# Performance work log

Hardware: AMD Instinct MI355X
Metric: run time of the kernel (lower is better)

Reference implementation:

```python
import jax, jax.numpy as jnp
import numpy as np
import math

B, S, D, H, FF = 2, 2048, 1024, 16, 4096
DH = D // H
EPS = 1e-5


def layernorm(x, g, b):
    mu = jnp.mean(x, axis=-1, keepdims=True)
    var = jnp.mean((x - mu) ** 2, axis=-1, keepdims=True)
    return (x - mu) * jax.lax.rsqrt(var + EPS) * g + b


def setup_inputs() -> dict:
    key = jax.random.key(0)
    ks = jax.random.split(key, 8)
    s = lambda fan_in: 1.0 / math.sqrt(fan_in)
    return {
        "x": jax.random.normal(ks[0], (B, S, D), jnp.float32),
        "attention_mask": jnp.zeros((B, 1, 1, S), jnp.float32),
        "wq": jax.random.uniform(ks[1], (D, D), jnp.float32, -s(D), s(D)),
        "wk": jax.random.uniform(ks[2], (D, D), jnp.float32, -s(D), s(D)),
        "wv": jax.random.uniform(ks[3], (D, D), jnp.float32, -s(D), s(D)),
        "wo": jax.random.uniform(ks[4], (D, D), jnp.float32, -s(D), s(D)),
        "w1": jax.random.uniform(ks[5], (D, FF), jnp.float32, -s(D), s(D)),
        "w2": jax.random.uniform(ks[6], (FF, D), jnp.float32, -s(FF), s(FF)),
        "ln1_g": jnp.ones((D,), jnp.float32),
        "ln1_b": jnp.zeros((D,), jnp.float32),
        "ln2_g": jnp.ones((D,), jnp.float32),
        "ln2_b": jnp.zeros((D,), jnp.float32),
    }


def reference(x, attention_mask, wq, wk, wv, wo, w1, w2, ln1_g, ln1_b, ln2_g, ln2_b):
    # --- attention ResNorm (pre-LN) ---
    y = layernorm(x, ln1_g, ln1_b)
    q = (y @ wq).reshape(B, S, H, DH)
    k = (y @ wk).reshape(B, S, H, DH)
    v = (y @ wv).reshape(B, S, H, DH)
    # NOTE: original scales by sqrt(hidden_dim), not sqrt(head_dim)
    scores = jnp.einsum("bqhd,bkhd->bhqk", q, k) / math.sqrt(D) + attention_mask
    probs = jax.nn.softmax(scores, axis=-1)
    attn = jnp.einsum("bhqk,bkhd->bqhd", probs, v).reshape(B, S, D)
    x = x + attn @ wo
    # --- FFN ResNorm ---
    y = layernorm(x, ln2_g, ln2_b)
    y = jax.nn.gelu(y @ w1, approximate=False) @ w2
    return x + y
```

## Files before the change

### kernel.cpp

```cpp
#include <hip/hip_runtime.h>
#include <hip/hip_bf16.h>
#include <math.h>

#define Bb 2
#define Ss 2048
#define Dd 1024
#define Hh 16
#define FFf 4096
#define EPSf 1e-5f
#define SCALEf 0.03125f
#define LOG2Ef 1.4426950408889634f
#define SCALE2f (SCALEf * LOG2Ef)
#define KSPLIT 2
#define NTILES ((Ss / KSPLIT) / 64)

typedef short s16x8 __attribute__((ext_vector_type(8)));
typedef short s16x4 __attribute__((ext_vector_type(4)));
typedef float f32x4 __attribute__((ext_vector_type(4)));
typedef float f32x16 __attribute__((ext_vector_type(16)));

__device__ __forceinline__ short f2bs(float f) {
    union { float f; unsigned u; } v; v.f = f;
    const unsigned r = (v.u + 0x7FFFu + ((v.u >> 16) & 1u)) >> 16;
    return (short)r;
}
__device__ __forceinline__ float bs2f(short s) {
    union { unsigned u; float f; } v; v.u = ((unsigned)(unsigned short)s) << 16;
    return v.f;
}
__device__ __forceinline__ float gelu_exact(float v) {
    return 0.5f * v * (1.0f + erff(v * 0.7071067811865475f));
}
__device__ __forceinline__ void gload16(const void* g, void* l) {
    __builtin_amdgcn_global_load_lds(
        (const __attribute__((address_space(1))) unsigned int*)g,
        (__attribute__((address_space(3))) unsigned int*)l, 16, 0, 0);
}
__device__ __forceinline__ unsigned cvt_pk(float lo, float hi) {
    unsigned r;
    asm("v_cvt_pk_bf16_f32 %0, %1, %2" : "=v"(r) : "v"(lo), "v"(hi));
    return r;
}

__global__ __launch_bounds__(256) void prep(const float* __restrict__ wq, const float* __restrict__ wk,
                                            const float* __restrict__ wv, const float* __restrict__ wo,
                                            const float* __restrict__ w1, const float* __restrict__ w2,
                                            const float* __restrict__ mask,
                                            short* __restrict__ qkvw_t, short* __restrict__ wot,
                                            short* __restrict__ w1t, short* __restrict__ w2t,
                                            float* __restrict__ msc) {
    const int blk = blockIdx.x;
    const int tid = threadIdx.x;
    if (blk >= 3072) {
#pragma unroll
        for (int j = 0; j < 16; ++j) msc[tid + j * 256] = mask[tid + j * 256] * LOG2Ef;
        return;
    }
    const float* W; short* Wt; int K, N, inner;
    if (blk < 1024) {
        const int which = blk >> 8; inner = blk & 255;
        K = 1024; N = 1024;
        W = (which == 0) ? wq : (which == 1) ? wk : (which == 2) ? wv : wo;
        Wt = (which < 3) ? qkvw_t + (size_t)which * 1024 * 1024 : wot;
    } else if (blk < 2048) {
        inner = blk - 1024; K = 1024; N = 4096; W = w1; Wt = w1t;
    } else {
        inner = blk - 2048; K = 4096; N = 1024; W = w2; Wt = w2t;
    }
    const int nbx = N / 64;
    const int bx = inner % nbx, by = inner / nbx;
    __shared__ short T[64][65];
    const int n0 = bx * 64, k0 = by * 64;
    const int c = tid & 63, rg = tid >> 6;
#pragma unroll
    for (int j = 0; j < 16; ++j) {
        const int r = rg * 16 + j;
        T[r][c] = f2bs(W[(size_t)(k0 + r) * N + n0 + c]);
    }
    __syncthreads();
#pragma unroll
    for (int j = 0; j < 16; ++j) {
        const int r = rg * 16 + j;
        Wt[(size_t)(n0 + r) * K + k0 + c] = T[c][r];
    }
}

__global__ __launch_bounds__(256) void vtranspose(const short* __restrict__ QKV,
                                                  short* __restrict__ VT) {
    __shared__ __align__(16) short T[64 * 144];
    const int t = threadIdx.x;
    const int bh = blockIdx.x;
    const int sc = blockIdx.y;
    const int b = bh >> 4, h = bh & 15;
#pragma unroll
    for (int i = 0; i < 4; ++i) {
        const int sl = i * 32 + (t >> 3);
        const int d0 = (t & 7) * 8;
        const s16x8 v = *(const s16x8*)&QKV[((size_t)(b * Ss + sc * 128 + sl)) * 3072 + 2048 + h * 64 + d0];
#pragma unroll
        for (int e = 0; e < 8; ++e) {
            const int d = d0 + e;
            T[(d * 144 + sl) ^ (((d >> 3) & 7) << 3)] = v[e];
        }
    }
    __syncthreads();
#pragma unroll
    for (int i = 0; i < 4; ++i) {
        const int d = i * 16 + (t >> 4);
        const int s0 = (t & 15) * 8;
        const s16x8 o = *(const s16x8*)&T[(d * 144 + s0) ^ (((d >> 3) & 7) << 3)];
        *(s16x8*)&VT[((size_t)(bh * 64 + d)) * 2048 + sc * 128 + s0] = o;
    }
}

__global__ __launch_bounds__(256) void layernorm_bf16(const float* __restrict__ X,
                                                      const float* __restrict__ g,
                                                      const float* __restrict__ bta,
                                                      short* __restrict__ Y) {
    __shared__ float red[8];
    const int row = blockIdx.x;
    const int tid = threadIdx.x;
    const size_t base = (size_t)row * Dd + tid * 4;
    const float4 xv = *(const float4*)&X[base];
    float s  = xv.x + xv.y + xv.z + xv.w;
    float sq = xv.x * xv.x + xv.y * xv.y + xv.z * xv.z + xv.w * xv.w;
#pragma unroll
    for (int o = 32; o >= 1; o >>= 1) {
        s  += __shfl_xor(s, o, 64);
        sq += __shfl_xor(sq, o, 64);
    }
    const int lane = tid & 63, wv = tid >> 6;
    if (lane == 0) { red[wv] = s; red[4 + wv] = sq; }
    __syncthreads();
    const float tot  = red[0] + red[1] + red[2] + red[3];
    const float totq = red[4] + red[5] + red[6] + red[7];
    const float mu  = tot * (1.0f / Dd);
    const float var = totq * (1.0f / Dd) - mu * mu;
    const float inv = 1.0f / sqrtf(var + EPSf);
    const float4 gv = *(const float4*)&g[tid * 4];
    const float4 bv = *(const float4*)&bta[tid * 4];
    s16x4 o;
    o[0] = f2bs((xv.x - mu) * inv * gv.x + bv.x);
    o[1] = f2bs((xv.y - mu) * inv * gv.y + bv.y);
    o[2] = f2bs((xv.z - mu) * inv * gv.z + bv.z);
    o[3] = f2bs((xv.w - mu) * inv * gv.w + bv.w);
    *(s16x4*)&Y[base] = o;
}

template <int BM, int BN, int BK, int EPI>
__global__ __launch_bounds__(256, 4) void gemm_v4(const short* __restrict__ A,
                                                  const short* __restrict__ Bt,
                                                  const float* __restrict__ R,
                                                  void* __restrict__ Cout,
                                                  int M, int N, int K, int gx) {
    constexpr int WM = BM / 2, WN = BN / 2;
    constexpr int MF = WM / 16, NF = WN / 16;
    constexpr int S   = BK / 8;
    constexpr int LPR = BK / 8;
    constexpr int RPI = 64 / LPR;
    constexpr int IPWA = (BM / 4) / RPI;
    constexpr int IPWB = (BN / 4) / RPI;
    __shared__ __align__(16) short As[2][BM * BK];
    __shared__ __align__(16) short Bs[2][BN * BK];

    const int tid = threadIdx.x;
    const int w = tid >> 6, l = tid & 63;
    const int lr = l & 15, lg = l >> 4;
    const int wr = w >> 1, wc = w & 1;

    const int nwg = gridDim.x;
    const int bid = blockIdx.x;
    const int swz = (bid & 7) * (nwg >> 3) + (bid >> 3);
    const int bx = swz % gx, by = swz / gx;

    const int lrow = l / LPR;
    const int sslot = ((l % LPR) ^ (((lrow * BK) >> 6) & (S - 1))) * 8;
    const size_t arow0 = (size_t)(by * BM);
    const size_t brow0 = (size_t)(bx * BN);

    f32x4 acc[NF][MF] = {};

    auto STAGE = [&](int bi, int k0) {
#pragma unroll
        for (int j = 0; j < IPWA; ++j) {
            const int r0 = w * (BM / 4) + j * RPI;
            gload16(A + (arow0 + r0 + lrow) * K + k0 + sslot, &As[bi][r0 * BK]);
        }
#pragma unroll
        for (int j = 0; j < IPWB; ++j) {
            const int r0 = w * (BN / 4) + j * RPI;
            gload16(Bt + (brow0 + r0 + lrow) * K + k0 + sslot, &Bs[bi][r0 * BK]);
        }
    };

    int aidx[2][MF], bidx[2][NF];
#pragma unroll
    for (int kk = 0; kk < BK / 32; ++kk) {
#pragma unroll
        for (int m = 0; m < MF; ++m) {
            const int r = wr * WM + m * 16 + lr;
            aidx[kk][m] = r * BK + ((kk * 4 + lg) ^ (((r * BK) >> 6) & (S - 1))) * 8;
        }
#pragma unroll
        for (int n = 0; n < NF; ++n) {
            const int r = wc * WN + n * 16 + lr;
            bidx[kk][n] = r * BK + ((kk * 4 + lg) ^ (((r * BK) >> 6) & (S - 1))) * 8;
        }
    }

    const int NKi = K / BK;
    STAGE(0, 0);

#pragma unroll 2
    for (int ks = 0; ks < NKi; ++ks) {
        const int cur = ks & 1;
        asm volatile("s_waitcnt vmcnt(0)" ::: "memory");
        __builtin_amdgcn_sched_barrier(0);
        __builtin_amdgcn_s_barrier();
        if (ks + 1 < NKi) STAGE(cur ^ 1, (ks + 1) * BK);

#pragma unroll
        for (int kk = 0; kk < BK / 32; ++kk) {
            s16x8 a[MF], b[NF];
#pragma unroll
            for (int m = 0; m < MF; ++m) a[m] = *(const s16x8*)&As[cur][aidx[kk][m]];
#pragma unroll
            for (int n = 0; n < NF; ++n) b[n] = *(const s16x8*)&Bs[cur][bidx[kk][n]];
            __builtin_amdgcn_s_setprio(1);
#pragma unroll
            for (int n = 0; n < NF; ++n)
#pragma unroll
                for (int m = 0; m < MF; ++m)
                    acc[n][m] = __builtin_amdgcn_mfma_f32_16x16x32_bf16(b[n], a[m], acc[n][m], 0, 0, 0);
            __builtin_amdgcn_s_setprio(0);
        }
    }

    const int row0 = by * BM + wr * WM;
    const int col0 = bx * BN + wc * WN;
#pragma unroll
    for (int m = 0; m < MF; ++m) {
        const int row = row0 + m * 16 + lr;
#pragma unroll
        for (int n = 0; n < NF; ++n) {
            const int cb = col0 + n * 16 + lg * 4;
            if (EPI == 2) {
                float* C = (float*)Cout;
                const f32x4 r4 = *(const f32x4*)&R[(size_t)row * N + cb];
                f32x4 o;
#pragma unroll
                for (int r = 0; r < 4; ++r) o[r] = acc[n][m][r] + r4[r];
                *(f32x4*)&C[(size_t)row * N + cb] = o;
            } else {
                s16x4 o;
#pragma unroll
                for (int r = 0; r < 4; ++r) {
                    float v = acc[n][m][r];
                    if (EPI == 1) v = gelu_exact(v);
                    o[r] = f2bs(v);
                }
                *(s16x4*)&((short*)Cout)[(size_t)row * N + cb] = o;
            }
        }
    }
}

__global__ __launch_bounds__(256, 4) void attn_split(const short* __restrict__ QKV,
                                                     const short* __restrict__ VT,
                                                     const float* __restrict__ MSC,
                                                     short* __restrict__ Opart,
                                                     float2* __restrict__ ML) {
    __shared__ __align__(16) short Kbuf[2][64 * 64];
    __shared__ __align__(16) short Vbuf[2][64 * 64];

    const int tid = threadIdx.x;
    const int w = tid >> 6, l = tid & 63;
    const int col = l & 31;
    const int hi = l >> 5;

    const int bid0 = blockIdx.x;
    const int bid = (bid0 & 7) * (gridDim.x >> 3) + (bid0 >> 3);
    const int part = bid >> 9;
    const int inner = bid & 511;
    const int qt = inner & 15, h = (inner >> 4) & 15, b = inner >> 8;
    const int q0 = qt * 128 + w * 32;
    const int k_base = part * (Ss / KSPLIT);

    s16x8 qf[4];
    {
        const short* qsrc = QKV + ((size_t)(b * Ss + q0 + col)) * 3072 + h * 64 + hi * 8;
        qf[0] = *(const s16x8*)(qsrc);
        qf[1] = *(const s16x8*)(qsrc + 16);
        qf[2] = *(const s16x8*)(qsrc + 32);
        qf[3] = *(const s16x8*)(qsrc + 48);
    }

    const int sr   = l >> 3;
    const int slot = ((l & 7) ^ (sr & 7)) * 8;
    const short* kg = QKV + (size_t)(b * Ss) * 3072 + 1024 + h * 64 + (size_t)sr * 3072 + slot;
    const short* vg = VT + ((size_t)(b * Hh + h) * 64 + sr) * 2048 + k_base + slot;
    const float* mscb = MSC + (size_t)b * Ss + k_base;

    int kidx[2][4], vidx[2][2][2];
#pragma unroll
    for (int sub = 0; sub < 2; ++sub) {
        const int rk = sub * 32 + col;
#pragma unroll
        for (int dd = 0; dd < 4; ++dd)
            kidx[sub][dd] = rk * 64 + ((2 * dd + hi) ^ (rk & 7)) * 8;
#pragma unroll
        for (int kk = 0; kk < 2; ++kk)
#pragma unroll
            for (int dt = 0; dt < 2; ++dt) {
                const int rv = dt * 32 + col;
                vidx[sub][kk][dt] = rv * 64 + ((sub * 4 + 2 * kk + hi) ^ (rv & 7)) * 8;
            }
    }

    f32x16 o_acc[2] = {};
    float m_used = -1e30f, l_run = 0.0f;

    auto STAGE = [&](int bi, int t) {
#pragma unroll
        for (int j = 0; j < 2; ++j) {
            const int r0 = w * 16 + j * 8;
            gload16(kg + (size_t)(k_base + t * 64 + r0) * 3072, &Kbuf[bi][r0 * 64]);
            gload16(vg + (size_t)r0 * 2048 + t * 64,             &Vbuf[bi][r0 * 64]);
        }
    };

    STAGE(0, 0);

#pragma unroll 2
    for (int i = 0; i < NTILES; ++i) {
        const int cur = i & 1;
        asm volatile("s_waitcnt vmcnt(0)" ::: "memory");
        __builtin_amdgcn_s_barrier();
        if (i + 1 < NTILES) STAGE(cur ^ 1, i + 1);

#pragma unroll
        for (int sub = 0; sub < 2; ++sub) {
            f32x16 sa = {};
#pragma unroll
            for (int dd = 0; dd < 4; ++dd) {
                const s16x8 kf = *(const s16x8*)&Kbuf[cur][kidx[sub][dd]];
                sa = __builtin_amdgcn_mfma_f32_32x32x16_bf16(kf, qf[dd], sa, 0, 0, 0);
            }

#pragma unroll
            for (int c4 = 0; c4 < 4; ++c4) {
                const f32x4 mv = *(const f32x4*)&mscb[i * 64 + sub * 32 + 8 * c4 + 4 * hi];
#pragma unroll
                for (int rr = 0; rr < 4; ++rr) sa[c4 * 4 + rr] = sa[c4 * 4 + rr] * SCALE2f + mv[rr];
            }
            float t8[8], t4[4];
#pragma unroll
            for (int r = 0; r < 8; ++r) t8[r] = fmaxf(sa[2 * r], sa[2 * r + 1]);
#pragma unroll
            for (int r = 0; r < 4; ++r) t4[r] = fmaxf(t8[2 * r], t8[2 * r + 1]);
            float tmax = fmaxf(fmaxf(t4[0], t4[1]), fmaxf(t4[2], t4[3]));
            {
                unsigned a = __float_as_uint(tmax), bq = __float_as_uint(tmax);
                asm volatile("v_permlane32_swap_b32 %0, %1" : "+v"(a), "+v"(bq));
                tmax = fmaxf(tmax, __uint_as_float(hi ? a : bq));
            }
            if (__any(tmax > m_used + 8.0f)) {
                const float nm = fmaxf(m_used, tmax);
                const float corr = __builtin_amdgcn_exp2f(m_used - nm);
                m_used = nm;
                l_run *= corr;
#pragma unroll
                for (int dt = 0; dt < 2; ++dt)
#pragma unroll
                    for (int r = 0; r < 16; ++r) o_acc[dt][r] *= corr;
            }

            unsigned wd[8];
            float s8[8];
#pragma unroll
            for (int m8 = 0; m8 < 8; ++m8) {
                const float p0 = __builtin_amdgcn_exp2f(sa[2 * m8]     - m_used);
                const float p1 = __builtin_amdgcn_exp2f(sa[2 * m8 + 1] - m_used);
                s8[m8] = p0 + p1;
                wd[m8] = cvt_pk(p0, p1);
            }
            float s4[4];
#pragma unroll
            for (int r = 0; r < 4; ++r) s4[r] = s8[2 * r] + s8[2 * r + 1];
            l_run += (s4[0] + s4[1]) + (s4[2] + s4[3]);

            unsigned f00 = wd[0], f02 = wd[2];
            asm volatile("v_permlane32_swap_b32 %0, %1" : "+v"(f00), "+v"(f02));
            unsigned f01 = wd[1], f03 = wd[3];
            asm volatile("v_permlane32_swap_b32 %0, %1" : "+v"(f01), "+v"(f03));
            unsigned f10 = wd[4], f12 = wd[6];
            asm volatile("v_permlane32_swap_b32 %0, %1" : "+v"(f10), "+v"(f12));
            unsigned f11 = wd[5], f13 = wd[7];
            asm volatile("v_permlane32_swap_b32 %0, %1" : "+v"(f11), "+v"(f13));
            union { unsigned u[4]; s16x8 v; } pf0, pf1;
            pf0.u[0] = f00; pf0.u[1] = f01; pf0.u[2] = f02; pf0.u[3] = f03;
            pf1.u[0] = f10; pf1.u[1] = f11; pf1.u[2] = f12; pf1.u[3] = f13;

#pragma unroll
            for (int dt = 0; dt < 2; ++dt) {
                const s16x8 v0 = *(const s16x8*)&Vbuf[cur][vidx[sub][0][dt]];
                const s16x8 v1 = *(const s16x8*)&Vbuf[cur][vidx[sub][1][dt]];
                o_acc[dt] = __builtin_amdgcn_mfma_f32_32x32x16_bf16(v0, pf0.v, o_acc[dt], 0, 0, 0);
                o_acc[dt] = __builtin_amdgcn_mfma_f32_32x32x16_bf16(v1, pf1.v, o_acc[dt], 0, 0, 0);
            }
        }
    }

    float l_tot;
    {
        unsigned a = __float_as_uint(l_run), bq = __float_as_uint(l_run);
        asm volatile("v_permlane32_swap_b32 %0, %1" : "+v"(a), "+v"(bq));
        l_tot = l_run + __uint_as_float(hi ? a : bq);
    }
    const size_t tok = (size_t)(b * Ss + q0 + col);
    if (hi == 0) {
        ML[(size_t)part * (Bb * Ss * Hh) + tok * Hh + h] = make_float2(m_used, l_tot);
    }
    short* obase = Opart + (size_t)part * (Bb * Ss) * Dd + tok * Dd + h * 64;
#pragma unroll
    for (int dt = 0; dt < 2; ++dt) {
#pragma unroll
        for (int c4 = 0; c4 < 4; ++c4) {
            s16x4 ov;
#pragma unroll
            for (int rr = 0; rr < 4; ++rr) ov[rr] = f2bs(o_acc[dt][c4 * 4 + rr]);
            *(s16x4*)&obase[dt * 32 + 8 * c4 + 4 * hi] = ov;
        }
    }
}

__global__ __launch_bounds__(256) void attn_combine(const short* __restrict__ Opart,
                                                    const float2* __restrict__ ML,
                                                    short* __restrict__ Oa) {
    const int tok = blockIdx.x;
    const int t = threadIdx.x;
    const int h = t >> 4;
    const int d = (t & 15) * 4;
    float2 ml[KSPLIT];
    float M = -1e30f;
#pragma unroll
    for (int p = 0; p < KSPLIT; ++p) {
        ml[p] = ML[(size_t)p * (Bb * Ss * Hh) + (size_t)tok * Hh + h];
        M = fmaxf(M, ml[p].x);
    }
    float a[KSPLIT], denom = 0.0f;
#pragma unroll
    for (int p = 0; p < KSPLIT; ++p) {
        a[p] = __builtin_amdgcn_exp2f(ml[p].x - M);
        denom += ml[p].y * a[p];
    }
    const float inv = 1.0f / denom;
    const size_t off = (size_t)tok * Dd + h * 64 + d;
    float acc[4] = {};
#pragma unroll
    for (int p = 0; p < KSPLIT; ++p) {
        const s16x4 o4 = *(const s16x4*)&Opart[(size_t)p * (Bb * Ss) * Dd + off];
#pragma unroll
        for (int r = 0; r < 4; ++r) acc[r] += bs2f(o4[r]) * a[p];
    }
    s16x4 o;
#pragma unroll
    for (int r = 0; r < 4; ++r) o[r] = f2bs(acc[r] * inv);
    *(s16x4*)&Oa[off] = o;
}

extern "C" void kernel_launch(void* const* d_in, const int* in_sizes, int n_in,
                              void* d_out, int out_size, void* d_ws, size_t ws_size,
                              hipStream_t stream) {
    const float* x    = (const float*)d_in[0];
    const float* mask = (const float*)d_in[1];
    const float* wq   = (const float*)d_in[2];
    const float* wk   = (const float*)d_in[3];
    const float* wv   = (const float*)d_in[4];
    const float* wo   = (const float*)d_in[5];
    const float* w1   = (const float*)d_in[6];
    const float* w2   = (const float*)d_in[7];
    const float* ln1g = (const float*)d_in[8];
    const float* ln1b = (const float*)d_in[9];
    const float* ln2g = (const float*)d_in[10];
    const float* ln2b = (const float*)d_in[11];
    float* out = (float*)d_out;

    char* p = (char*)d_ws;
    short* qkvw_t = (short*)p; p += (size_t)3072 * 1024 * 2;
    short* wot    = (short*)p; p += (size_t)1024 * 1024 * 2;
    short* w1t    = (short*)p; p += (size_t)4096 * 1024 * 2;
    short* w2t    = (short*)p; p += (size_t)1024 * 4096 * 2;
    short* y_bf   = (short*)p; p += (size_t)4096 * 1024 * 2;
    short* qkv    = (short*)p; p += (size_t)4096 * 3072 * 2;
    short* attn_b = (short*)p; p += (size_t)4096 * 1024 * 2;
    short* y2_bf  = (short*)p; p += (size_t)4096 * 1024 * 2;
    char*  hregion = p;        p += (size_t)4096 * 4096 * 2;
    float* msc    = (float*)p; p += (size_t)Bb * Ss * 4;

    short*  h_bf   = (short*)hregion;
    short*  o_part = (short*)hregion;
    short*  vt     = y_bf;
    float2* ml     = (float2*)qkvw_t;

    const int M = Bb * Ss;

    prep<<<3073, 256, 0, stream>>>(wq, wk, wv, wo, w1, w2, mask, qkvw_t, wot, w1t, w2t, msc);
    layernorm_bf16<<<M, 256, 0, stream>>>(x, ln1g, ln1b, y_bf);
    gemm_v4<128, 128, 32, 0><<<768, 256, 0, stream>>>(y_bf, qkvw_t, nullptr, qkv, M, 3072, 1024, 24);
    vtranspose<<<dim3(32, 16), 256, 0, stream>>>(qkv, vt);
    attn_split<<<KSPLIT * 512, 256, 0, stream>>>(qkv, vt, msc, o_part, ml);
    attn_combine<<<M, 256, 0, stream>>>(o_part, ml, attn_b);
    gemm_v4<64, 64, 32, 2><<<1024, 256, 0, stream>>>(attn_b, wot, x, out, M, 1024, 1024, 16);
    layernorm_bf16<<<M, 256, 0, stream>>>(out, ln2g, ln2b, y2_bf);
    gemm_v4<128, 128, 32, 1><<<1024, 256, 0, stream>>>(y2_bf, w1t, nullptr, h_bf, M, 4096, 1024, 32);
    gemm_v4<64, 64, 32, 2><<<1024, 256, 0, stream>>>(h_bf, w2t, out, out, M, 1024, 4096, 16);
}
```

Before: 262.1 us.

## Add 256x256 eight-wave GEMM with phased LDS pipeline for QKV and FFN1

Adds a new GEMM kernel with 256x256 output tiles, 512 threads and a K step of 64 split into two 32-wide halves. The halves are double-buffered and loaded in staggered phases, so global loads overlap the MFMA work with partial waitcnt. It replaces the 128x128 gemm_v4 for the QKV projection and the FFN up-projection to raise data reuse per tile. It also strips setprio and sched_barrier from gemm_v4, which is still used for the other GEMMs. The larger tiles leave fewer workgroups (192 and 256) across the CUs, which risks poor load balance.

```diff
diff --git a/kernel.cpp b/kernel.cpp
--- a/kernel.cpp
+++ b/kernel.cpp
@@ -147,6 +147,158 @@
     *(s16x4*)&Y[base] = o;
 }
 
+template <int EPI>
+__global__ __launch_bounds__(512, 2) void gemm_8ph(const short* __restrict__ A,
+                                                   const short* __restrict__ Bt,
+                                                   void* __restrict__ Cout,
+                                                   int M, int N, int K, int gx) {
+    __shared__ __align__(16) short As[2][2][256 * 32];
+    __shared__ __align__(16) short Bs[2][2][256 * 32];
+
+    const int tid = threadIdx.x;
+    const int w = tid >> 6, l = tid & 63;
+    const int lr = l & 15, lg = l >> 4;
+    const int wr = w >> 2, wc = w & 3;
+
+    const int nwg = gridDim.x;
+    const int bid = blockIdx.x;
+    const int swz = (bid & 7) * (nwg >> 3) + (bid >> 3);
+    const int bx = swz % gx, by = swz / gx;
+
+    const int srow  = l >> 2;
+    const int sslot = ((l & 3) ^ ((l >> 3) & 3)) * 8;
+    const size_t arow0 = (size_t)by * 256;
+    const size_t brow0 = (size_t)bx * 256;
+
+    const int fq   = (lg ^ ((lr >> 1) & 3)) * 8;
+    const int aoff = (wr * 128 + lr) * 32 + fq;
+    const int boff = (wc * 64 + lr) * 32 + fq;
+
+    f32x4 acc[8][4] = {};
+
+    auto STAGE_A = [&](int bi, int kk, int ks) {
+        const int kcol = ks * 64 + kk * 32;
+#pragma unroll
+        for (int j = 0; j < 2; ++j) {
+            const int r0 = w * 32 + j * 16;
+            gload16(A + (arow0 + r0 + srow) * K + kcol + sslot, &As[bi][kk][r0 * 32]);
+        }
+    };
+    auto STAGE_B = [&](int bi, int kk, int ks) {
+        const int kcol = ks * 64 + kk * 32;
+#pragma unroll
+        for (int j = 0; j < 2; ++j) {
+            const int r0 = w * 32 + j * 16;
+            gload16(Bt + (brow0 + r0 + srow) * K + kcol + sslot, &Bs[bi][kk][r0 * 32]);
+        }
+    };
+
+    const int NK = K / 64;
+    STAGE_A(0, 0, 0); STAGE_B(0, 0, 0); STAGE_A(0, 1, 0); STAGE_B(0, 1, 0);
+
+#pragma unroll 2
+    for (int ks = 0; ks < NK; ++ks) {
+        const int cur = ks & 1, nxt = cur ^ 1;
+        const bool more = (ks + 1 < NK);
+
+        asm volatile("s_waitcnt vmcnt(4)" ::: "memory");
+        __builtin_amdgcn_s_barrier();
+        s16x8 b0 = *(const s16x8*)&Bs[cur][0][boff];
+        s16x8 b1 = *(const s16x8*)&Bs[cur][0][boff + 512];
+        s16x8 b2 = *(const s16x8*)&Bs[cur][0][boff + 1024];
+        s16x8 b3 = *(const s16x8*)&Bs[cur][0][boff + 1536];
+        s16x8 a0 = *(const s16x8*)&As[cur][0][aoff];
+        s16x8 a1 = *(const s16x8*)&As[cur][0][aoff + 512];
+        s16x8 a2 = *(const s16x8*)&As[cur][0][aoff + 1024];
+        s16x8 a3 = *(const s16x8*)&As[cur][0][aoff + 1536];
+        if (more) STAGE_A(nxt, 0, ks + 1);
+        __builtin_amdgcn_s_setprio(1);
+#pragma unroll
+        for (int n = 0; n < 4; ++n) {
+            const s16x8 bn = (n == 0) ? b0 : (n == 1) ? b1 : (n == 2) ? b2 : b3;
+            acc[0][n] = __builtin_amdgcn_mfma_f32_16x16x32_bf16(bn, a0, acc[0][n], 0, 0, 0);
+            acc[1][n] = __builtin_amdgcn_mfma_f32_16x16x32_bf16(bn, a1, acc[1][n], 0, 0, 0);
+            acc[2][n] = __builtin_amdgcn_mfma_f32_16x16x32_bf16(bn, a2, acc[2][n], 0, 0, 0);
+            acc[3][n] = __builtin_amdgcn_mfma_f32_16x16x32_bf16(bn, a3, acc[3][n], 0, 0, 0);
+        }
+        __builtin_amdgcn_s_setprio(0);
+
+        s16x8 a4 = *(const s16x8*)&As[cur][0][aoff + 2048];
+        s16x8 a5 = *(const s16x8*)&As[cur][0][aoff + 2560];
+        s16x8 a6 = *(const s16x8*)&As[cur][0][aoff + 3072];
+        s16x8 a7 = *(const s16x8*)&As[cur][0][aoff + 3584];
+        if (more) STAGE_B(nxt, 0, ks + 1);
+        __builtin_amdgcn_s_setprio(1);
+#pragma unroll
+        for (int n = 0; n < 4; ++n) {
+            const s16x8 bn = (n == 0) ? b0 : (n == 1) ? b1 : (n == 2) ? b2 : b3;
+            acc[4][n] = __builtin_amdgcn_mfma_f32_16x16x32_bf16(bn, a4, acc[4][n], 0, 0, 0);
+            acc[5][n] = __builtin_amdgcn_mfma_f32_16x16x32_bf16(bn, a5, acc[5][n], 0, 0, 0);
+            acc[6][n] = __builtin_amdgcn_mfma_f32_16x16x32_bf16(bn, a6, acc[6][n], 0, 0, 0);
+            acc[7][n] = __builtin_amdgcn_mfma_f32_16x16x32_bf16(bn, a7, acc[7][n], 0, 0, 0);
+        }
+        __builtin_amdgcn_s_setprio(0);
+
+        if (more) { asm volatile("s_waitcnt vmcnt(4)" ::: "memory"); }
+        else      { asm volatile("s_waitcnt vmcnt(0)" ::: "memory"); }
+        __builtin_amdgcn_s_barrier();
+        b0 = *(const s16x8*)&Bs[cur][1][boff];
+        b1 = *(const s16x8*)&Bs[cur][1][boff + 512];
+        b2 = *(const s16x8*)&Bs[cur][1][boff + 1024];
+        b3 = *(const s16x8*)&Bs[cur][1][boff + 1536];
+        a0 = *(const s16x8*)&As[cur][1][aoff];
+        a1 = *(const s16x8*)&As[cur][1][aoff + 512];
+        a2 = *(const s16x8*)&As[cur][1][aoff + 1024];
+        a3 = *(const s16x8*)&As[cur][1][aoff + 1536];
+        if (more) STAGE_A(nxt, 1, ks + 1);
+        __builtin_amdgcn_s_setprio(1);
+#pragma unroll
+        for (int n = 0; n < 4; ++n) {
+            const s16x8 bn = (n == 0) ? b0 : (n == 1) ? b1 : (n == 2) ? b2 : b3;
+            acc[0][n] = __builtin_amdgcn_mfma_f32_16x16x32_bf16(bn, a0, acc[0][n], 0, 0, 0);
+            acc[1][n] = __builtin_amdgcn_mfma_f32_16x16x32_bf16(bn, a1, acc[1][n], 0, 0, 0);
+            acc[2][n] = __builtin_amdgcn_mfma_f32_16x16x32_bf16(bn, a2, acc[2][n], 0, 0, 0);
+            acc[3][n] = __builtin_amdgcn_mfma_f32_16x16x32_bf16(bn, a3, acc[3][n], 0, 0, 0);
+        }
+        __builtin_amdgcn_s_setprio(0);
+
+        a4 = *(const s16x8*)&As[cur][1][aoff + 2048];
+        a5 = *(const s16x8*)&As[cur][1][aoff + 2560];
+        a6 = *(const s16x8*)&As[cur][1][aoff + 3072];
+        a7 = *(const s16x8*)&As[cur][1][aoff + 3584];
+        if (more) STAGE_B(nxt, 1, ks + 1);
+        __builtin_amdgcn_s_setprio(1);
+#pragma unroll
+        for (int n = 0; n < 4; ++n) {
+            const s16x8 bn = (n == 0) ? b0 : (n == 1) ? b1 : (n == 2) ? b2 : b3;
+            acc[4][n] = __builtin_amdgcn_mfma_f32_16x16x32_bf16(bn, a4, acc[4][n], 0, 0, 0);
+            acc[5][n] = __builtin_amdgcn_mfma_f32_16x16x32_bf16(bn, a5, acc[5][n], 0, 0, 0);
+            acc[6][n] = __builtin_amdgcn_mfma_f32_16x16x32_bf16(bn, a6, acc[6][n], 0, 0, 0);
+            acc[7][n] = __builtin_amdgcn_mfma_f32_16x16x32_bf16(bn, a7, acc[7][n], 0, 0, 0);
+        }
+        __builtin_amdgcn_s_setprio(0);
+    }
+
+    const int row0 = by * 256 + wr * 128;
+    const int col0 = bx * 256 + wc * 64;
+#pragma unroll
+    for (int m = 0; m < 8; ++m) {
+        const int row = row0 + m * 16 + lr;
+#pragma unroll
+        for (int n = 0; n < 4; ++n) {
+            const int cb = col0 + n * 16 + lg * 4;
+            s16x4 o;
+#pragma unroll
+            for (int r = 0; r < 4; ++r) {
+                float v = acc[m][n][r];
+                if (EPI == 1) v = gelu_exact(v);
+                o[r] = f2bs(v);
+            }
+            *(s16x4*)&((short*)Cout)[(size_t)row * N + cb] = o;
+        }
+    }
+}
+
 template <int BM, int BN, int BK, int EPI>
 __global__ __launch_bounds__(256, 4) void gemm_v4(const short* __restrict__ A,
                                                   const short* __restrict__ Bt,
@@ -193,7 +345,7 @@
         }
     };
 
-    int aidx[2][MF], bidx[2][NF];
+    int aidx[BK / 32][MF], bidx[BK / 32][NF];
 #pragma unroll
     for (int kk = 0; kk < BK / 32; ++kk) {
 #pragma unroll
@@ -215,7 +367,6 @@
     for (int ks = 0; ks < NKi; ++ks) {
         const int cur = ks & 1;
         asm volatile("s_waitcnt vmcnt(0)" ::: "memory");
-        __builtin_amdgcn_sched_barrier(0);
         __builtin_amdgcn_s_barrier();
         if (ks + 1 < NKi) STAGE(cur ^ 1, (ks + 1) * BK);
 
@@ -226,13 +377,11 @@
             for (int m = 0; m < MF; ++m) a[m] = *(const s16x8*)&As[cur][aidx[kk][m]];
 #pragma unroll
             for (int n = 0; n < NF; ++n) b[n] = *(const s16x8*)&Bs[cur][bidx[kk][n]];
-            __builtin_amdgcn_s_setprio(1);
 #pragma unroll
             for (int n = 0; n < NF; ++n)
 #pragma unroll
                 for (int m = 0; m < MF; ++m)
                     acc[n][m] = __builtin_amdgcn_mfma_f32_16x16x32_bf16(b[n], a[m], acc[n][m], 0, 0, 0);
-            __builtin_amdgcn_s_setprio(0);
         }
     }
 
@@ -507,12 +656,12 @@
 
     prep<<<3073, 256, 0, stream>>>(wq, wk, wv, wo, w1, w2, mask, qkvw_t, wot, w1t, w2t, msc);
     layernorm_bf16<<<M, 256, 0, stream>>>(x, ln1g, ln1b, y_bf);
-    gemm_v4<128, 128, 32, 0><<<768, 256, 0, stream>>>(y_bf, qkvw_t, nullptr, qkv, M, 3072, 1024, 24);
+    gemm_8ph<0><<<192, 512, 0, stream>>>(y_bf, qkvw_t, qkv, M, 3072, 1024, 12);
     vtranspose<<<dim3(32, 16), 256, 0, stream>>>(qkv, vt);
     attn_split<<<KSPLIT * 512, 256, 0, stream>>>(qkv, vt, msc, o_part, ml);
     attn_combine<<<M, 256, 0, stream>>>(o_part, ml, attn_b);
     gemm_v4<64, 64, 32, 2><<<1024, 256, 0, stream>>>(attn_b, wot, x, out, M, 1024, 1024, 16);
     layernorm_bf16<<<M, 256, 0, stream>>>(out, ln2g, ln2b, y2_bf);
-    gemm_v4<128, 128, 32, 1><<<1024, 256, 0, stream>>>(y2_bf, w1t, nullptr, h_bf, M, 4096, 1024, 32);
+    gemm_8ph<1><<<256, 512, 0, stream>>>(y2_bf, w1t, h_bf, M, 4096, 1024, 16);
     gemm_v4<64, 64, 32, 2><<<1024, 256, 0, stream>>>(h_bf, w2t, out, out, M, 1024, 4096, 16);
 }
```

Result: no change. 267.2 us (+2.0%).
